# Performance work log

Hardware: AMD Instinct MI355X
Metric: run time of the kernel (lower is better)

The kernel has to match this reference:

```python
import jax, jax.numpy as jnp
import numpy as np

N_NODES = 250_000
N_EDGES = 4_000_000


def setup_inputs() -> dict:
    key = jax.random.key(0)
    ks = jax.random.split(key, 8)
    x = jax.random.normal(ks[0], (N_NODES, 3), dtype=jnp.float32)
    w = jax.random.normal(ks[1], (N_EDGES, 4), dtype=jnp.float32)
    # MLP params: Linear(10->40), ReLU, Linear(40->4); torch Linear layout [out, in]
    W1 = jax.random.normal(ks[2], (40, 10), dtype=jnp.float32) * (1.0 / np.sqrt(10.0))
    b1 = jax.random.normal(ks[3], (40,), dtype=jnp.float32) * 0.01
    W2 = jax.random.normal(ks[4], (4, 40), dtype=jnp.float32) * (1.0 / np.sqrt(40.0))
    b2 = jax.random.normal(ks[5], (4,), dtype=jnp.float32) * 0.01
    src = jax.random.randint(ks[6], (N_EDGES,), 0, N_NODES, dtype=jnp.int64)
    dst = jax.random.randint(ks[7], (N_EDGES,), 0, N_NODES, dtype=jnp.int64)
    return {"x": x, "w": w, "W1": W1, "b1": b1, "W2": W2, "b2": b2,
            "src": src, "dst": dst}


def reference(x, w, W1, b1, W2, b2, src, dst):
    x_src = x[src]                                  # [E, 3] gather
    x_dst = x[dst]                                  # [E, 3] gather
    m = jnp.concatenate([x_src, x_dst, w], axis=1)  # [E, 10]
    h = jax.nn.relu(m @ W1.T + b1)                  # [E, 40]
    w_out = h @ W2.T + b2                           # [E, 4]
    e_tilde = jnp.concatenate([x_src, w_out], axis=1)  # [E, 7]
    return w_out, e_tilde
```

## Files before the change

### kernel.cpp

```cpp
#include <hip/hip_runtime.h>

typedef __fp16 h2 __attribute__((ext_vector_type(2)));
typedef float f4 __attribute__((ext_vector_type(4)));

static __device__ __forceinline__ unsigned pkrtz(float a, float b) {
    union { h2 v; unsigned u; } cv;
    cv.v = __builtin_amdgcn_cvt_pkrtz(a, b);
    return cv.u;
}
static __device__ __forceinline__ h2 as_h2(unsigned u) {
    union { unsigned u; h2 v; } cv; cv.u = u; return cv.v;
}

__global__ void prep_kernel(const float* __restrict__ W1, const float* __restrict__ b1,
                            const float* __restrict__ W2, const float* __restrict__ b2,
                            unsigned* __restrict__ ws) {
    const int t = threadIdx.x;
    if (t < 40) {
        #pragma unroll
        for (int i = 0; i < 5; ++i)
            ws[t * 6 + i] = pkrtz(W1[t * 10 + 2 * i], W1[t * 10 + 2 * i + 1]);
        ws[t * 6 + 5] = __float_as_uint(b1[t]);
    } else if (t < 60) {
        const int p = t - 40;
        #pragma unroll
        for (int o = 0; o < 4; ++o)
            ws[240 + p * 4 + o] = pkrtz(W2[o * 40 + 2 * p], W2[o * 40 + 2 * p + 1]);
    } else if (t < 64) {
        ws[320 + (t - 60)] = __float_as_uint(b2[t - 60]);
    }
}

#define TPB 256

__global__ __launch_bounds__(TPB) void edge_mlp_nt_kernel(
    const float* __restrict__ x,
    const float* __restrict__ w,
    const int* __restrict__ src,
    const int* __restrict__ dst,
    const unsigned* __restrict__ W,
    float* __restrict__ w_out,
    float* __restrict__ e_tilde,
    int E)
{
    __shared__ float s_et[4][64 * 7];

    const int t    = threadIdx.x;
    const int wave = t >> 6;
    const int lane = t & 63;
    const int e    = blockIdx.x * TPB + t;

    float m0 = 0.f, m1 = 0.f, m2 = 0.f;
    h2 vm0 = as_h2(0), vm1 = as_h2(0), vm2 = as_h2(0), vm3 = as_h2(0), vm4 = as_h2(0);

    if (e < E) {
        const int si = __builtin_nontemporal_load(src + e);
        const int di = __builtin_nontemporal_load(dst + e);
        m0 = x[3 * si]; m1 = x[3 * si + 1]; m2 = x[3 * si + 2];
        const float d0 = x[3 * di], d1 = x[3 * di + 1], d2 = x[3 * di + 2];
        const f4 wv = __builtin_nontemporal_load((const f4*)w + e);
        vm0 = as_h2(pkrtz(m0, m1));
        vm1 = as_h2(pkrtz(m2, d0));
        vm2 = as_h2(pkrtz(d1, d2));
        vm3 = as_h2(pkrtz(wv.x, wv.y));
        vm4 = as_h2(pkrtz(wv.z, wv.w));
    }

    float o0 = __uint_as_float(W[320]);
    float o1 = __uint_as_float(W[321]);
    float o2 = __uint_as_float(W[322]);
    float o3 = __uint_as_float(W[323]);

    #pragma unroll
    for (int jp = 0; jp < 20; ++jp) {
        const int j0 = 2 * jp, j1 = 2 * jp + 1;
        float h0v = __uint_as_float(W[j0 * 6 + 5]);
        float h1v = __uint_as_float(W[j1 * 6 + 5]);
        h0v = __builtin_amdgcn_fdot2(vm0, as_h2(W[j0 * 6 + 0]), h0v, false);
        h1v = __builtin_amdgcn_fdot2(vm0, as_h2(W[j1 * 6 + 0]), h1v, false);
        h0v = __builtin_amdgcn_fdot2(vm1, as_h2(W[j0 * 6 + 1]), h0v, false);
        h1v = __builtin_amdgcn_fdot2(vm1, as_h2(W[j1 * 6 + 1]), h1v, false);
        h0v = __builtin_amdgcn_fdot2(vm2, as_h2(W[j0 * 6 + 2]), h0v, false);
        h1v = __builtin_amdgcn_fdot2(vm2, as_h2(W[j1 * 6 + 2]), h1v, false);
        h0v = __builtin_amdgcn_fdot2(vm3, as_h2(W[j0 * 6 + 3]), h0v, false);
        h1v = __builtin_amdgcn_fdot2(vm3, as_h2(W[j1 * 6 + 3]), h1v, false);
        h0v = __builtin_amdgcn_fdot2(vm4, as_h2(W[j0 * 6 + 4]), h0v, false);
        h1v = __builtin_amdgcn_fdot2(vm4, as_h2(W[j1 * 6 + 4]), h1v, false);
        h0v = fmaxf(h0v, 0.f);
        h1v = fmaxf(h1v, 0.f);
        const h2 hp = as_h2(pkrtz(h0v, h1v));
        o0 = __builtin_amdgcn_fdot2(hp, as_h2(W[240 + jp * 4 + 0]), o0, false);
        o1 = __builtin_amdgcn_fdot2(hp, as_h2(W[240 + jp * 4 + 1]), o1, false);
        o2 = __builtin_amdgcn_fdot2(hp, as_h2(W[240 + jp * 4 + 2]), o2, false);
        o3 = __builtin_amdgcn_fdot2(hp, as_h2(W[240 + jp * 4 + 3]), o3, false);
    }

    if (e < E) {
        f4 ov; ov.x = o0; ov.y = o1; ov.z = o2; ov.w = o3;
        __builtin_nontemporal_store(ov, (f4*)w_out + e);
    }

    float* sw = s_et[wave];
    sw[lane * 7 + 0] = m0;
    sw[lane * 7 + 1] = m1;
    sw[lane * 7 + 2] = m2;
    sw[lane * 7 + 3] = o0;
    sw[lane * 7 + 4] = o1;
    sw[lane * 7 + 5] = o2;
    sw[lane * 7 + 6] = o3;
    __syncthreads();

    const int base_e  = blockIdx.x * TPB + wave * 64;
    const int nvalid  = (E - base_e < 64 ? (E - base_e) : 64) * 7;
    const long long fbase = (long long)base_e * 7;
    #pragma unroll
    for (int k = 0; k < 7; ++k) {
        const int idx = lane + 64 * k;
        if (idx < nvalid)
            __builtin_nontemporal_store(sw[idx], e_tilde + fbase + idx);
    }
}

extern "C" void kernel_launch(void* const* d_in, const int* in_sizes, int n_in,
                              void* d_out, int out_size, void* d_ws, size_t ws_size,
                              hipStream_t stream) {
    const float* x  = (const float*)d_in[0];
    const float* w  = (const float*)d_in[1];
    const float* W1 = (const float*)d_in[2];
    const float* b1 = (const float*)d_in[3];
    const float* W2 = (const float*)d_in[4];
    const float* b2 = (const float*)d_in[5];
    const int* src  = (const int*)d_in[6];
    const int* dst  = (const int*)d_in[7];

    const int E = in_sizes[6];

    float* w_out   = (float*)d_out;
    float* e_tilde = w_out + (size_t)E * 4;
    unsigned* ws   = (unsigned*)d_ws;

    prep_kernel<<<1, 64, 0, stream>>>(W1, b1, W2, b2, ws);

    const int nblocks = (E + TPB - 1) / TPB;
    edge_mlp_nt_kernel<<<nblocks, TPB, 0, stream>>>(
        x, w, src, dst, ws, w_out, e_tilde, E);
}
```

Baseline: 98.47 us.

## Pre-pack node features to fp16 pairs and vectorize e_tilde stores

A new pre-kernel converts x into 8-byte rows of packed fp16 values, so each edge gathers its source and destination with a single load each instead of three scalar float loads. The packed halves are reassembled with byte permutes into the dot-product operands. The block-wide barrier is dropped because each wave only uses its own shared-memory slice. Full waves now write e_tilde with 16-byte vector stores. The trade-offs are one extra small launch and x_src in e_tilde now being fp16-rounded rather than exact.

Result: slower. 106.6 us (+8.2%).

```diff
diff --git a/kernel.cpp b/kernel.cpp
--- a/kernel.cpp
+++ b/kernel.cpp
@@ -2,6 +2,7 @@
 
 typedef __fp16 h2 __attribute__((ext_vector_type(2)));
 typedef float f4 __attribute__((ext_vector_type(4)));
+typedef unsigned u2 __attribute__((ext_vector_type(2)));
 
 static __device__ __forceinline__ unsigned pkrtz(float a, float b) {
     union { h2 v; unsigned u; } cv;
@@ -31,10 +32,21 @@
     }
 }
 
+__global__ __launch_bounds__(256) void pack_x_kernel(const float* __restrict__ x,
+                                                     u2* __restrict__ xh, int N) {
+    const int i = blockIdx.x * 256 + threadIdx.x;
+    if (i < N) {
+        u2 v;
+        v.x = pkrtz(x[3 * i], x[3 * i + 1]);
+        v.y = pkrtz(x[3 * i + 2], 0.f);
+        __builtin_nontemporal_store(v, xh + i);
+    }
+}
+
 #define TPB 256
 
-__global__ __launch_bounds__(TPB) void edge_mlp_nt_kernel(
-    const float* __restrict__ x,
+__global__ __launch_bounds__(TPB) void edge_mlp_h16_kernel(
+    const u2* __restrict__ xh,
     const float* __restrict__ w,
     const int* __restrict__ src,
     const int* __restrict__ dst,
@@ -56,14 +68,15 @@
     if (e < E) {
         const int si = __builtin_nontemporal_load(src + e);
         const int di = __builtin_nontemporal_load(dst + e);
-        m0 = x[3 * si]; m1 = x[3 * si + 1]; m2 = x[3 * si + 2];
-        const float d0 = x[3 * di], d1 = x[3 * di + 1], d2 = x[3 * di + 2];
+        const u2 sv = xh[si];
+        const u2 dv = xh[di];
         const f4 wv = __builtin_nontemporal_load((const f4*)w + e);
-        vm0 = as_h2(pkrtz(m0, m1));
-        vm1 = as_h2(pkrtz(m2, d0));
-        vm2 = as_h2(pkrtz(d1, d2));
+        vm0 = as_h2(sv.x);
+        vm1 = as_h2(__builtin_amdgcn_perm(sv.y, dv.x, 0x01000504u));
+        vm2 = as_h2(__builtin_amdgcn_perm(dv.x, dv.y, 0x01000706u));
         vm3 = as_h2(pkrtz(wv.x, wv.y));
         vm4 = as_h2(pkrtz(wv.z, wv.w));
+        m0 = (float)vm0.x; m1 = (float)vm0.y; m2 = (float)as_h2(sv.y).x;
     }
 
     float o0 = __uint_as_float(W[320]);
@@ -108,16 +121,30 @@
     sw[lane * 7 + 4] = o1;
     sw[lane * 7 + 5] = o2;
     sw[lane * 7 + 6] = o3;
-    __syncthreads();
 
-    const int base_e  = blockIdx.x * TPB + wave * 64;
-    const int nvalid  = (E - base_e < 64 ? (E - base_e) : 64) * 7;
+    const int base_e = blockIdx.x * TPB + wave * 64;
     const long long fbase = (long long)base_e * 7;
-    #pragma unroll
-    for (int k = 0; k < 7; ++k) {
-        const int idx = lane + 64 * k;
-        if (idx < nvalid)
-            __builtin_nontemporal_store(sw[idx], e_tilde + fbase + idx);
+    if (base_e + 64 <= E) {
+        f4* dst4 = (f4*)(e_tilde + fbase);
+        {
+            f4 v0; v0.x = sw[4 * lane]; v0.y = sw[4 * lane + 1];
+            v0.z = sw[4 * lane + 2]; v0.w = sw[4 * lane + 3];
+            __builtin_nontemporal_store(v0, dst4 + lane);
+        }
+        if (lane < 48) {
+            const int i2 = 64 + lane;
+            f4 v1; v1.x = sw[4 * i2]; v1.y = sw[4 * i2 + 1];
+            v1.z = sw[4 * i2 + 2]; v1.w = sw[4 * i2 + 3];
+            __builtin_nontemporal_store(v1, dst4 + i2);
+        }
+    } else {
+        const int nvalid = (E - base_e < 64 ? (E - base_e) : 64) * 7;
+        #pragma unroll
+        for (int k = 0; k < 7; ++k) {
+            const int idx = lane + 64 * k;
+            if (idx < nvalid)
+                __builtin_nontemporal_store(sw[idx], e_tilde + fbase + idx);
+        }
     }
 }
 
@@ -134,6 +161,7 @@
     const int* dst  = (const int*)d_in[7];
 
     const int E = in_sizes[6];
+    const int N = in_sizes[0] / 3;
 
     float* w_out   = (float*)d_out;
     float* e_tilde = w_out + (size_t)E * 4;
@@ -141,7 +169,11 @@
 
     prep_kernel<<<1, 64, 0, stream>>>(W1, b1, W2, b2, ws);
 
+    const size_t pack_off = 4096;
+    u2* xh = (u2*)((char*)d_ws + pack_off);
+    pack_x_kernel<<<(N + 255) / 256, 256, 0, stream>>>(x, xh, N);
+
     const int nblocks = (E + TPB - 1) / TPB;
-    edge_mlp_nt_kernel<<<nblocks, TPB, 0, stream>>>(
-        x, w, src, dst, ws, w_out, e_tilde, E);
+    edge_mlp_h16_kernel<<<nblocks, TPB, 0, stream>>>(
+        xh, w, src, dst, ws, w_out, e_tilde, E);
 }
```
